# Kernel optimization log

Measured on AMD Instinct MI355X. Metric: run time of the kernel, lower is better.

The kernel has to match this reference:

```python
import jax, jax.numpy as jnp
import numpy as np

N = 100000      # nodes
E = 3200000     # directed edges
F_IN = 128      # input node features
H = 16          # hidden width (fixed by module code)
C = 40          # classes
K_HOPS = 10
ALPHA = 0.1
BN_EPS = 1e-5


def gcn_conv(x, W, b, src, dst, n):
    """PyG GCNConv: add self-loops, symmetric D^-1/2 (A+I) D^-1/2 aggregation of x@W, plus bias."""
    loop = jnp.arange(n)
    s = jnp.concatenate([src, loop])
    d = jnp.concatenate([dst, loop])
    deg = jax.ops.segment_sum(jnp.ones(s.shape[0], x.dtype), d, num_segments=n)
    dinv = jnp.where(deg > 0, jax.lax.rsqrt(deg), 0.0)
    norm = dinv[s] * dinv[d]                      # [E+N]
    h = x @ W                                     # [N, out]
    out = jax.ops.segment_sum(h[s] * norm[:, None], d, num_segments=n)
    return out + b


def setup_inputs() -> dict:
    key = jax.random.key(0)
    ks = jax.random.split(key, 6)
    x = jax.random.normal(ks[0], (N, F_IN), jnp.float32)
    src = jax.random.randint(ks[1], (E,), 0, N)
    dst = jax.random.randint(ks[2], (E,), 0, N)
    glorot = lambda k, sh, fan: jax.random.normal(k, sh, jnp.float32) * np.float32(1.0 / np.sqrt(fan))
    W1 = glorot(ks[3], (F_IN, H), F_IN)
    b1 = jnp.zeros((H,), jnp.float32)
    gamma = jnp.ones((H,), jnp.float32)
    beta = jnp.zeros((H,), jnp.float32)
    Wl = glorot(ks[4], (H, H), H)
    bl = jnp.zeros((H,), jnp.float32)
    W2 = glorot(ks[5], (H, C), H)
    b2 = jnp.zeros((C,), jnp.float32)
    return dict(x=x, src=src, dst=dst, W1=W1, b1=b1, gamma=gamma, beta=beta,
                Wl=Wl, bl=bl, W2=W2, b2=b2)


def reference(x, src, dst, W1, b1, gamma, beta, Wl, bl, W2, b2):
    h = jax.nn.relu(gcn_conv(x, W1, b1, src, dst, N))
    # BatchNorm1d in training mode: biased batch statistics over nodes
    mean = h.mean(axis=0)
    var = h.var(axis=0)
    h = (h - mean) * jax.lax.rsqrt(var + BN_EPS) * gamma + beta
    # k_hops iterations of tiny linear-relu-residual blend
    def step(h, _):
        return ALPHA * jax.nn.relu(h @ Wl + bl) + (1.0 - ALPHA) * h, None
    h, _ = jax.lax.scan(step, h, None, length=K_HOPS)
    out = gcn_conv(h, W2, b2, src, dst, N)
    return jax.nn.log_softmax(out, axis=1)
```

## Files before the change

kernel.cpp:

```cpp
#include <hip/hip_runtime.h>
#include <hip/hip_fp16.h>
#include <math.h>

#define F_IN 128
#define H 16
#define C 40
#define K_HOPS 10
#define ALPHA 0.1f
#define BN_EPS 1e-5f

#define RB 256
#define RB_BITS 8
#define NBKT_MAX 512
#define SRC_MASK 0x1FFFF
#define PADQ 16
#define NDUMMY 2048
#define CAPB_BITS 14
#define CAPB (1 << CAPB_BITS)
#define STAGE_CAP 14336

typedef int v4i __attribute__((ext_vector_type(4)));

__global__ void k_zero(int* __restrict__ gcur, float* __restrict__ stats,
                       __half* __restrict__ h1h, __half* __restrict__ hh, int n) {
    int id = blockIdx.x * blockDim.x + threadIdx.x;
    if (id < NBKT_MAX) gcur[id] = id << CAPB_BITS;
    if (id < 32) stats[id] = 0.0f;
    int* z1 = (int*)(h1h + (size_t)n * H);
    int* z2 = (int*)(hh + (size_t)n * H);
    if (id < NDUMMY * H / 2) { z1[id] = 0; z2[id] = 0; }
}

#define BIN_CHUNK 4096
__global__ __launch_bounds__(512) void k_bin(const int* __restrict__ src,
                                             const int* __restrict__ dst,
                                             int* __restrict__ gcur,
                                             int* __restrict__ temp, int e) {
    __shared__ int hist[NBKT_MAX];
    __shared__ int cur[NBKT_MAX];
    __shared__ int gofs[NBKT_MAX];
    __shared__ int wsum[8];
    __shared__ int stageV[BIN_CHUNK];
    __shared__ int stageD[BIN_CHUNK];
    int t = threadIdx.x;
    hist[t] = 0;
    __syncthreads();
    int base = blockIdx.x * BIN_CHUNK;
    int cnt = e - base; if (cnt > BIN_CHUNK) cnt = BIN_CHUNK;
    const v4i* s4 = reinterpret_cast<const v4i*>(src + base);
    const v4i* d4 = reinterpret_cast<const v4i*>(dst + base);
    v4i sv[2], dv[2];
#pragma unroll
    for (int i = 0; i < 2; ++i) {
        int e0 = (t * 2 + i) * 4;
        if (e0 + 3 < cnt) { sv[i] = s4[t * 2 + i]; dv[i] = d4[t * 2 + i]; }
        else if (e0 < cnt) {
            int ts[4], td[4];
#pragma unroll
            for (int j = 0; j < 4; ++j) {
                int ei = e0 + j;
                ts[j] = (ei < cnt) ? src[base + ei] : 0;
                td[j] = (ei < cnt) ? dst[base + ei] : -1;
            }
            sv[i] = *reinterpret_cast<v4i*>(ts); dv[i] = *reinterpret_cast<v4i*>(td);
        } else { dv[i] = (v4i){-1, -1, -1, -1}; sv[i] = dv[i]; }
    }
#pragma unroll
    for (int i = 0; i < 2; ++i) {
        if (dv[i].x >= 0) atomicAdd(&hist[dv[i].x >> RB_BITS], 1);
        if (dv[i].y >= 0) atomicAdd(&hist[dv[i].y >> RB_BITS], 1);
        if (dv[i].z >= 0) atomicAdd(&hist[dv[i].z >> RB_BITS], 1);
        if (dv[i].w >= 0) atomicAdd(&hist[dv[i].w >> RB_BITS], 1);
    }
    __syncthreads();
    int v = hist[t];
    int lane = t & 63, wv = t >> 6;
    int s = v;
#pragma unroll
    for (int off = 1; off < 64; off <<= 1) { int u = __shfl_up(s, off); if (lane >= off) s += u; }
    if (lane == 63) wsum[wv] = s;
    __syncthreads();
    if (t < 8) {
        int x = wsum[t];
#pragma unroll
        for (int off = 1; off < 8; off <<= 1) { int u = __shfl_up(x, off); if (t >= off) x += u; }
        wsum[t] = x;
    }
    __syncthreads();
    int excl = s - v + (wv ? wsum[wv - 1] : 0);
    cur[t] = excl;
    int g = v ? atomicAdd(&gcur[t], v) : 0;
    gofs[t] = g - excl;
    __syncthreads();
#pragma unroll
    for (int i = 0; i < 2; ++i) {
        int ds[4] = { dv[i].x, dv[i].y, dv[i].z, dv[i].w };
        int ssx[4] = { sv[i].x, sv[i].y, sv[i].z, sv[i].w };
#pragma unroll
        for (int j = 0; j < 4; ++j) {
            int d = ds[j];
            if (d >= 0) {
                int b = d >> RB_BITS;
                int pos = atomicAdd(&cur[b], 1);
                stageV[pos] = ssx[j] | ((d & (RB - 1)) << 17);
                stageD[pos] = gofs[b];
            }
        }
    }
    __syncthreads();
    for (int i = t; i < cnt; i += 512)
        temp[stageD[i] + i] = stageV[i];
}

__global__ __launch_bounds__(512) void k_sort(const int* __restrict__ gcur,
                                              const int* __restrict__ temp,
                                              int* __restrict__ csr,
                                              int* __restrict__ ostart,
                                              int* __restrict__ oend,
                                              int* __restrict__ onode,
                                              float* __restrict__ dinv, int n) {
    __shared__ int hist[RB];
    __shared__ int cur[RB];
    __shared__ int wsum[4];
    __shared__ int qh[64];
    __shared__ int qb[64];
    __shared__ int ptotS;
    __shared__ int stage[STAGE_CAP];
    int t = threadIdx.x;
    int bkt = blockIdx.x;
    int start = bkt << CAPB_BITS;
    int endi = gcur[bkt];
    int nv = endi - start;
    int n4 = nv >> 2;
    const v4i* t4 = reinterpret_cast<const v4i*>(temp + start);
    if (t < RB) hist[t] = 0;
    if (t < 64) qh[t] = 0;
    __syncthreads();
    for (int k = t; k < n4; k += 512) {
        v4i v = t4[k];
        atomicAdd(&hist[v.x >> 17], 1);
        atomicAdd(&hist[v.y >> 17], 1);
        atomicAdd(&hist[v.z >> 17], 1);
        atomicAdd(&hist[v.w >> 17], 1);
    }
    for (int k = start + (n4 << 2) + t; k < endi; k += 512)
        atomicAdd(&hist[temp[k] >> 17], 1);
    __syncthreads();
    int node = (bkt << RB_BITS) + t;
    int h = 0, pv = 0;
    bool va = false;
    if (t < RB) {
        h = hist[t];
        pv = (h + PADQ - 1) & ~(PADQ - 1);
        va = (node < n);
        if (va) dinv[node] = rsqrtf((float)(h + 1));
    }
    int lane = t & 63, wv = t >> 6;
    int s = pv;
#pragma unroll
    for (int off = 1; off < 64; off <<= 1) { int u = __shfl_up(s, off); if (lane >= off) s += u; }
    if (lane == 63 && wv < 4) wsum[wv] = s;
    __syncthreads();
    if (t < 4) {
        int x = wsum[t];
#pragma unroll
        for (int off = 1; off < 4; off <<= 1) { int u = __shfl_up(x, off); if (t >= off) x += u; }
        wsum[t] = x;
        if (t == 3) ptotS = x;
    }
    __syncthreads();
    int pexcl = 0, s0 = 0, q = 63, r = 0;
    if (t < RB) {
        pexcl = s - pv + (wv ? wsum[wv - 1] : 0);
        s0 = start + pexcl;
        q = 63 - min(pv >> 4, 63);
        r = atomicAdd(&qh[q], 1);
    }
    __syncthreads();
    int ptotal = ptotS;
    if (t == 0) {
        int run = 0;
        for (int i = 0; i < 64; ++i) { qb[i] = run; run += qh[i]; }
    }
    __syncthreads();
    if (t < RB) {
        int ga = (bkt << RB_BITS) + qb[q] + r;
        ostart[ga] = s0; oend[ga] = s0 + pv; onode[ga] = va ? node : -1;
    }
    if (ptotal <= STAGE_CAP) {
        if (t < RB) cur[t] = pexcl;
        for (int i = t; i < ptotal; i += 512) stage[i] = -1;
        __syncthreads();
        for (int k = t; k < n4; k += 512) {
            v4i v = t4[k];
            int p0 = atomicAdd(&cur[v.x >> 17], 1); stage[p0] = v.x & SRC_MASK;
            int p1 = atomicAdd(&cur[v.y >> 17], 1); stage[p1] = v.y & SRC_MASK;
            int p2 = atomicAdd(&cur[v.z >> 17], 1); stage[p2] = v.z & SRC_MASK;
            int p3 = atomicAdd(&cur[v.w >> 17], 1); stage[p3] = v.w & SRC_MASK;
        }
        for (int k = start + (n4 << 2) + t; k < endi; k += 512) {
            int v = temp[k];
            int pos = atomicAdd(&cur[v >> 17], 1);
            stage[pos] = v & SRC_MASK;
        }
        __syncthreads();
        for (int i = t * 4; i < ptotal; i += 2048) {
            v4i v = *reinterpret_cast<const v4i*>(&stage[i]);
            int gi = start + i;
            v.x = (v.x < 0) ? n + ((gi + 0) & (NDUMMY - 1)) : v.x;
            v.y = (v.y < 0) ? n + ((gi + 1) & (NDUMMY - 1)) : v.y;
            v.z = (v.z < 0) ? n + ((gi + 2) & (NDUMMY - 1)) : v.z;
            v.w = (v.w < 0) ? n + ((gi + 3) & (NDUMMY - 1)) : v.w;
            *reinterpret_cast<v4i*>(&csr[gi]) = v;
        }
    } else {
        if (t < RB) cur[t] = s0;
        __syncthreads();
        for (int k = start + t; k < endi; k += 512) {
            int v = temp[k];
            int pos = atomicAdd(&cur[v >> 17], 1);
            csr[pos] = v & SRC_MASK;
        }
        __syncthreads();
        if (t < RB) for (int i = s0 + h; i < s0 + pv; ++i) csr[i] = n + (i & (NDUMMY - 1));
    }
}

__global__ __launch_bounds__(256) void k_mm1(const float* __restrict__ x,
                                             const float* __restrict__ W1,
                                             const float* __restrict__ dinv,
                                             __half* __restrict__ h1h, int n) {
    __shared__ __align__(16) float xs[16 * 132];
    __shared__ __align__(16) float ws[128 * 16];
    int t = threadIdx.x;
    int node0 = blockIdx.x * 16;
    const float4* x4 = reinterpret_cast<const float4*>(x);
    const float4* w4 = reinterpret_cast<const float4*>(W1);
#pragma unroll
    for (int r = 0; r < 2; ++r) {
        int f = t + r * 256;
        int nl = f >> 5, k4 = f & 31;
        int nn = node0 + nl; if (nn >= n) nn = n - 1;
        *reinterpret_cast<float4*>(&xs[nl * 132 + k4 * 4]) = x4[(size_t)nn * 32 + k4];
        *reinterpret_cast<float4*>(&ws[f * 4]) = w4[f];
    }
    __syncthreads();
    int nl = t >> 4, j = t & 15;
    float acc = 0.0f;
#pragma unroll 8
    for (int k = 0; k < 128; ++k)
        acc = fmaf(xs[nl * 132 + k], ws[k * 16 + j], acc);
    int node = node0 + nl;
    if (node < n) h1h[(size_t)node * H + j] = __float2half(acc * dinv[node]);
}

__device__ __forceinline__ void acc8(float* a, int4 gv) {
    const __half2* h = reinterpret_cast<const __half2*>(&gv);
    float2 f0 = __half22float2(h[0]);
    float2 f1 = __half22float2(h[1]);
    float2 f2 = __half22float2(h[2]);
    float2 f3 = __half22float2(h[3]);
    a[0] += f0.x; a[1] += f0.y; a[2] += f1.x; a[3] += f1.y;
    a[4] += f2.x; a[5] += f2.y; a[6] += f3.x; a[7] += f3.y;
}

__global__ __launch_bounds__(256) void k_gather1(const int* __restrict__ ostart,
                                                 const int* __restrict__ oend,
                                                 const int* __restrict__ onode,
                                                 const int* __restrict__ csr,
                                                 const __half* __restrict__ h1h,
                                                 const float* __restrict__ dinv,
                                                 const float* __restrict__ b1,
                                                 float* __restrict__ hout,
                                                 float* __restrict__ stats, int n) {
    __shared__ float sm[32];
    __shared__ float b1s[16];
    int t = threadIdx.x;
    if (t < 32) sm[t] = 0.0f;
    if (t < 16) b1s[t] = b1[t];
    __syncthreads();
    int idx = blockIdx.x * 256 + t;
    int g = idx >> 2;
    int L = idx & 3, p = L >> 1, jj = L & 1;
    int node = __builtin_nontemporal_load(onode + g);
    float a[8];
#pragma unroll
    for (int k = 0; k < 8; ++k) a[k] = 0.0f;
    const int4* tab = reinterpret_cast<const int4*>(h1h);
    if (node >= 0) {
        int c  = (__builtin_nontemporal_load(ostart + g) >> 2) + (p << 1);
        int ce = __builtin_nontemporal_load(oend + g) >> 2;
        const v4i* csr4 = reinterpret_cast<const v4i*>(csr);
        for (; c < ce; c += 4) {
            v4i e0 = __builtin_nontemporal_load(csr4 + c);
            v4i e1 = __builtin_nontemporal_load(csr4 + c + 1);
            int4 g0 = tab[(size_t)e0.x * 2 + jj];
            int4 g1 = tab[(size_t)e0.y * 2 + jj];
            int4 g2 = tab[(size_t)e0.z * 2 + jj];
            int4 g3 = tab[(size_t)e0.w * 2 + jj];
            int4 g4 = tab[(size_t)e1.x * 2 + jj];
            int4 g5 = tab[(size_t)e1.y * 2 + jj];
            int4 g6 = tab[(size_t)e1.z * 2 + jj];
            int4 g7 = tab[(size_t)e1.w * 2 + jj];
            acc8(a, g0); acc8(a, g1); acc8(a, g2); acc8(a, g3);
            acc8(a, g4); acc8(a, g5); acc8(a, g6); acc8(a, g7);
        }
    }
#pragma unroll
    for (int k = 0; k < 8; ++k) a[k] += __shfl_xor(a[k], 2);
    float din = 0.0f;
    int4 sv = make_int4(0, 0, 0, 0);
    if (node >= 0) {
        din = dinv[node];
        sv = tab[(size_t)node * 2 + jj];
    }
    float v[8];
    {
        const __half2* h = reinterpret_cast<const __half2*>(&sv);
        float2 f0 = __half22float2(h[0]), f1 = __half22float2(h[1]);
        float2 f2 = __half22float2(h[2]), f3 = __half22float2(h[3]);
        float s8[8] = { f0.x, f0.y, f1.x, f1.y, f2.x, f2.y, f3.x, f3.y };
        bool writer = (node >= 0) && (p == 0);
#pragma unroll
        for (int k = 0; k < 8; ++k) {
            float val = fmaxf(din * (a[k] + s8[k]) + b1s[jj * 8 + k], 0.0f);
            v[k] = writer ? val : 0.0f;
        }
        if (writer) {
            float4* o = reinterpret_cast<float4*>(hout + (size_t)node * H + jj * 8);
            o[0] = make_float4(v[0], v[1], v[2], v[3]);
            o[1] = make_float4(v[4], v[5], v[6], v[7]);
        }
    }
#pragma unroll
    for (int k = 0; k < 8; ++k) {
        float s1 = v[k], s2 = v[k] * v[k];
        s1 += __shfl_xor(s1, 2);  s2 += __shfl_xor(s2, 2);
        s1 += __shfl_xor(s1, 4);  s2 += __shfl_xor(s2, 4);
        s1 += __shfl_xor(s1, 8);  s2 += __shfl_xor(s2, 8);
        s1 += __shfl_xor(s1, 16); s2 += __shfl_xor(s2, 16);
        s1 += __shfl_xor(s1, 32); s2 += __shfl_xor(s2, 32);
        if ((t & 63) < 2) {
            atomicAdd(&sm[jj * 8 + k], s1);
            atomicAdd(&sm[16 + jj * 8 + k], s2);
        }
    }
    __syncthreads();
    if (t < 32) atomicAdd(&stats[t], sm[t]);
}

__global__ __launch_bounds__(256) void k_hops(const float* __restrict__ h,
                                              __half* __restrict__ hh,
                                              const float* __restrict__ stats,
                                              const float* __restrict__ gamma,
                                              const float* __restrict__ beta,
                                              const float* __restrict__ Wl,
                                              const float* __restrict__ bl,
                                              const float* __restrict__ dinv, int n, float nf) {
    __shared__ float wl[256], bls[16], av[16], cv[16];
    int t = threadIdx.x;
    wl[t] = Wl[(t & 15) * 16 + (t >> 4)];
    if (t < 16) {
        bls[t] = bl[t];
        float mean = stats[t] / nf;
        float var = stats[16 + t] / nf - mean * mean;
        float aa = gamma[t] * rsqrtf(var + BN_EPS);
        av[t] = aa;
        cv[t] = beta[t] - mean * aa;
    }
    __syncthreads();
    int node = blockIdx.x * 256 + t;
    if (node >= n) return;
    float hr[16];
    {
        const float4* hp = reinterpret_cast<const float4*>(h + (size_t)node * H);
        float4 v0 = hp[0], v1 = hp[1], v2 = hp[2], v3 = hp[3];
        hr[0] = v0.x; hr[1] = v0.y; hr[2] = v0.z; hr[3] = v0.w;
        hr[4] = v1.x; hr[5] = v1.y; hr[6] = v1.z; hr[7] = v1.w;
        hr[8] = v2.x; hr[9] = v2.y; hr[10] = v2.z; hr[11] = v2.w;
        hr[12] = v3.x; hr[13] = v3.y; hr[14] = v3.z; hr[15] = v3.w;
    }
#pragma unroll
    for (int j = 0; j < 16; ++j) hr[j] = hr[j] * av[j] + cv[j];
    for (int it = 0; it < K_HOPS; ++it) {
        float tmp[16];
#pragma unroll
        for (int j = 0; j < 16; ++j) {
            float a = bls[j];
#pragma unroll
            for (int k = 0; k < 16; ++k) a = fmaf(hr[k], wl[j * 16 + k], a);
            tmp[j] = fmaxf(a, 0.0f);
        }
#pragma unroll
        for (int j = 0; j < 16; ++j) hr[j] = ALPHA * tmp[j] + (1.0f - ALPHA) * hr[j];
    }
    {
        float din = dinv[node];
        __half2 ph[8];
#pragma unroll
        for (int i = 0; i < 8; ++i)
            ph[i] = __floats2half2_rn(hr[2 * i] * din, hr[2 * i + 1] * din);
        int4* hp = reinterpret_cast<int4*>(hh + (size_t)node * H);
        hp[0] = *reinterpret_cast<int4*>(&ph[0]);
        hp[1] = *reinterpret_cast<int4*>(&ph[4]);
    }
}

__global__ __launch_bounds__(256) void k_g2f(const int* __restrict__ ostart,
                                             const int* __restrict__ oend,
                                             const int* __restrict__ onode,
                                             const int* __restrict__ csr,
                                             const __half* __restrict__ hh,
                                             const float* __restrict__ dinv,
                                             const float* __restrict__ W2,
                                             const float* __restrict__ b2,
                                             float* __restrict__ out, int n) {
    __shared__ __align__(16) float w2t[40 * 20];
    __shared__ float b2s[40];
    __shared__ __align__(16) float feat[64 * 20];
    int t = threadIdx.x;
    for (int i = t; i < 640; i += 256) w2t[(i >> 4) * 20 + (i & 15)] = W2[(i & 15) * 40 + (i >> 4)];
    if (t < 40) b2s[t] = b2[t];
    int idx = blockIdx.x * 256 + t;
    int g = idx >> 2;
    int L = idx & 3, p = L >> 1, jj = L & 1;
    int node = __builtin_nontemporal_load(onode + g);
    float a[8];
#pragma unroll
    for (int k = 0; k < 8; ++k) a[k] = 0.0f;
    const int4* tab = reinterpret_cast<const int4*>(hh);
    if (node >= 0) {
        int c  = (__builtin_nontemporal_load(ostart + g) >> 2) + (p << 1);
        int ce = __builtin_nontemporal_load(oend + g) >> 2;
        const v4i* csr4 = reinterpret_cast<const v4i*>(csr);
        for (; c < ce; c += 4) {
            v4i e0 = __builtin_nontemporal_load(csr4 + c);
            v4i e1 = __builtin_nontemporal_load(csr4 + c + 1);
            int4 g0 = tab[(size_t)e0.x * 2 + jj];
            int4 g1 = tab[(size_t)e0.y * 2 + jj];
            int4 g2 = tab[(size_t)e0.z * 2 + jj];
            int4 g3 = tab[(size_t)e0.w * 2 + jj];
            int4 g4 = tab[(size_t)e1.x * 2 + jj];
            int4 g5 = tab[(size_t)e1.y * 2 + jj];
            int4 g6 = tab[(size_t)e1.z * 2 + jj];
            int4 g7 = tab[(size_t)e1.w * 2 + jj];
            acc8(a, g0); acc8(a, g1); acc8(a, g2); acc8(a, g3);
            acc8(a, g4); acc8(a, g5); acc8(a, g6); acc8(a, g7);
        }
    }
#pragma unroll
    for (int k = 0; k < 8; ++k) a[k] += __shfl_xor(a[k], 2);
    int nl = t >> 2;
    if (node >= 0 && p == 0) {
        float din = dinv[node];
        int4 sv = tab[(size_t)node * 2 + jj];
        const __half2* h = reinterpret_cast<const __half2*>(&sv);
        float2 f0 = __half22float2(h[0]), f1 = __half22float2(h[1]);
        float2 f2 = __half22float2(h[2]), f3 = __half22float2(h[3]);
        float s8[8] = { f0.x, f0.y, f1.x, f1.y, f2.x, f2.y, f3.x, f3.y };
        float v[8];
#pragma unroll
        for (int k = 0; k < 8; ++k) v[k] = din * (a[k] + s8[k]);
        *reinterpret_cast<float4*>(&feat[nl * 20 + jj * 8])     = make_float4(v[0], v[1], v[2], v[3]);
        *reinterpret_cast<float4*>(&feat[nl * 20 + jj * 8 + 4]) = make_float4(v[4], v[5], v[6], v[7]);
    }
    __syncthreads();
    float4 f0 = *reinterpret_cast<const float4*>(&feat[nl * 20]);
    float4 f1 = *reinterpret_cast<const float4*>(&feat[nl * 20 + 4]);
    float4 f2 = *reinterpret_cast<const float4*>(&feat[nl * 20 + 8]);
    float4 f3 = *reinterpret_cast<const float4*>(&feat[nl * 20 + 12]);
    int cb = (t & 3) * 10;
    float z[10];
#pragma unroll
    for (int j = 0; j < 10; ++j) {
        const float4* wr = reinterpret_cast<const float4*>(&w2t[(cb + j) * 20]);
        float4 w0 = wr[0], w1 = wr[1], w2v = wr[2], w3 = wr[3];
        float acc = b2s[cb + j];
        acc = fmaf(f0.x, w0.x, acc); acc = fmaf(f0.y, w0.y, acc);
        acc = fmaf(f0.z, w0.z, acc); acc = fmaf(f0.w, w0.w, acc);
        acc = fmaf(f1.x, w1.x, acc); acc = fmaf(f1.y, w1.y, acc);
        acc = fmaf(f1.z, w1.z, acc); acc = fmaf(f1.w, w1.w, acc);
        acc = fmaf(f2.x, w2v.x, acc); acc = fmaf(f2.y, w2v.y, acc);
        acc = fmaf(f2.z, w2v.z, acc); acc = fmaf(f2.w, w2v.w, acc);
        acc = fmaf(f3.x, w3.x, acc); acc = fmaf(f3.y, w3.y, acc);
        acc = fmaf(f3.z, w3.z, acc); acc = fmaf(f3.w, w3.w, acc);
        z[j] = acc;
    }
    float m = z[0];
#pragma unroll
    for (int j = 1; j < 10; ++j) m = fmaxf(m, z[j]);
    m = fmaxf(m, __shfl_xor(m, 1));
    m = fmaxf(m, __shfl_xor(m, 2));
    float s = 0.0f;
#pragma unroll
    for (int j = 0; j < 10; ++j) s += expf(z[j] - m);
    s += __shfl_xor(s, 1);
    s += __shfl_xor(s, 2);
    float lse = m + logf(s);
    if (node >= 0) {
        float2* o = reinterpret_cast<float2*>(out + (size_t)node * 40 + cb);
#pragma unroll
        for (int j = 0; j < 5; ++j)
            o[j] = make_float2(z[2 * j] - lse, z[2 * j + 1] - lse);
    }
}

extern "C" void kernel_launch(void* const* d_in, const int* in_sizes, int n_in,
                              void* d_out, int out_size, void* d_ws, size_t ws_size,
                              hipStream_t stream) {
    const float* x     = (const float*)d_in[0];
    const int*   src   = (const int*)d_in[1];
    const int*   dst   = (const int*)d_in[2];
    const float* W1    = (const float*)d_in[3];
    const float* b1    = (const float*)d_in[4];
    const float* gamma = (const float*)d_in[5];
    const float* beta  = (const float*)d_in[6];
    const float* Wl    = (const float*)d_in[7];
    const float* bl    = (const float*)d_in[8];
    const float* W2    = (const float*)d_in[9];
    const float* b2    = (const float*)d_in[10];
    float* out = (float*)d_out;

    int n = in_sizes[0] / F_IN;
    int e = in_sizes[1];
    int nbkt = (n + RB - 1) >> RB_BITS;
    int nAlign = (n + 15) & ~15;
    int nG = nbkt * RB;
    size_t bktB = (size_t)nbkt << CAPB_BITS;
    size_t hTileB = (size_t)nAlign * H * 4;
    size_t unionB = bktB * 4;
    if (unionB < hTileB) unionB = hTileB;

    char* wsb = (char*)d_ws;
    int*    csr      = (int*)wsb;      wsb += (bktB + 64) * 4;
    char*   uni      = wsb;            wsb += unionB;
    int*    temp     = (int*)uni;
    float*  hbuf     = (float*)uni;
    int*    ostart   = (int*)wsb;      wsb += (size_t)(nG + 16) * 4;
    int*    oend     = (int*)wsb;      wsb += (size_t)(nG + 16) * 4;
    int*    onode    = (int*)wsb;      wsb += (size_t)(nG + 16) * 4;
    float*  dinv     = (float*)wsb;    wsb += (size_t)nAlign * 4;
    int*    gcur     = (int*)wsb;      wsb += NBKT_MAX * 4;
    float*  stats    = (float*)wsb;    wsb += 64 * 4;
    __half* h1h      = (__half*)wsb;   wsb += (size_t)(nAlign + NDUMMY + 16) * H * 2;
    __half* hh       = (__half*)wsb;   wsb += (size_t)(nAlign + NDUMMY + 16) * H * 2;

    k_zero<<<64, 256, 0, stream>>>(gcur, stats, h1h, hh, n);
    k_bin<<<(e + BIN_CHUNK - 1) / BIN_CHUNK, 512, 0, stream>>>(src, dst, gcur, temp, e);
    k_sort<<<nbkt, 512, 0, stream>>>(gcur, temp, csr, ostart, oend, onode, dinv, n);
    k_mm1<<<(n + 15) / 16, 256, 0, stream>>>(x, W1, dinv, h1h, n);
    k_gather1<<<nbkt * 4, 256, 0, stream>>>(ostart, oend, onode, csr, h1h, dinv, b1, hbuf, stats, n);
    k_hops<<<(n + 255) / 256, 256, 0, stream>>>(hbuf, hh, stats, gamma, beta, Wl, bl, dinv, n, (float)n);
    k_g2f<<<nbkt * 4, 256, 0, stream>>>(ostart, oend, onode, csr, hh, dinv, W2, b2, out, n);
}
```

Before: 261.1 us.

## Use persistent grid-stride blocks and prefetch CSR indices in gather kernels

Both gather kernels now launch a fixed grid of 512 blocks that loop over node groups with a grid stride, instead of one block per 64-node group. In the first gather, BN statistics are accumulated in registers across iterations and reduced once per block, which cuts shared and global atomics. The CSR index loads are software-prefetched one iteration ahead so they overlap the feature gathers. k_g2f double-buffers its shared feature tile so only one barrier is needed per iteration. The risks are lower occupancy or load imbalance with only 512 blocks, and extra register pressure from the prefetch.

Result: no change. 264.0 us (+1.1%).

```diff
diff --git a/kernel.cpp b/kernel.cpp
--- a/kernel.cpp
+++ b/kernel.cpp
@@ -18,6 +18,7 @@
 #define CAPB_BITS 14
 #define CAPB (1 << CAPB_BITS)
 #define STAGE_CAP 14336
+#define GR 512
 
 typedef int v4i __attribute__((ext_vector_type(4)));
 
@@ -272,69 +273,78 @@
                                                  const float* __restrict__ dinv,
                                                  const float* __restrict__ b1,
                                                  float* __restrict__ hout,
-                                                 float* __restrict__ stats, int n) {
+                                                 float* __restrict__ stats, int nG, int n) {
     __shared__ float sm[32];
     __shared__ float b1s[16];
     int t = threadIdx.x;
     if (t < 32) sm[t] = 0.0f;
     if (t < 16) b1s[t] = b1[t];
     __syncthreads();
-    int idx = blockIdx.x * 256 + t;
-    int g = idx >> 2;
-    int L = idx & 3, p = L >> 1, jj = L & 1;
-    int node = __builtin_nontemporal_load(onode + g);
-    float a[8];
-#pragma unroll
-    for (int k = 0; k < 8; ++k) a[k] = 0.0f;
+    int L = t & 3, p = L >> 1, jj = L & 1;
     const int4* tab = reinterpret_cast<const int4*>(h1h);
-    if (node >= 0) {
-        int c  = (__builtin_nontemporal_load(ostart + g) >> 2) + (p << 1);
-        int ce = __builtin_nontemporal_load(oend + g) >> 2;
-        const v4i* csr4 = reinterpret_cast<const v4i*>(csr);
-        for (; c < ce; c += 4) {
-            v4i e0 = __builtin_nontemporal_load(csr4 + c);
-            v4i e1 = __builtin_nontemporal_load(csr4 + c + 1);
-            int4 g0 = tab[(size_t)e0.x * 2 + jj];
-            int4 g1 = tab[(size_t)e0.y * 2 + jj];
-            int4 g2 = tab[(size_t)e0.z * 2 + jj];
-            int4 g3 = tab[(size_t)e0.w * 2 + jj];
-            int4 g4 = tab[(size_t)e1.x * 2 + jj];
-            int4 g5 = tab[(size_t)e1.y * 2 + jj];
-            int4 g6 = tab[(size_t)e1.z * 2 + jj];
-            int4 g7 = tab[(size_t)e1.w * 2 + jj];
-            acc8(a, g0); acc8(a, g1); acc8(a, g2); acc8(a, g3);
-            acc8(a, g4); acc8(a, g5); acc8(a, g6); acc8(a, g7);
-        }
-    }
-#pragma unroll
-    for (int k = 0; k < 8; ++k) a[k] += __shfl_xor(a[k], 2);
-    float din = 0.0f;
-    int4 sv = make_int4(0, 0, 0, 0);
-    if (node >= 0) {
-        din = dinv[node];
-        sv = tab[(size_t)node * 2 + jj];
-    }
-    float v[8];
-    {
-        const __half2* h = reinterpret_cast<const __half2*>(&sv);
-        float2 f0 = __half22float2(h[0]), f1 = __half22float2(h[1]);
-        float2 f2 = __half22float2(h[2]), f3 = __half22float2(h[3]);
-        float s8[8] = { f0.x, f0.y, f1.x, f1.y, f2.x, f2.y, f3.x, f3.y };
-        bool writer = (node >= 0) && (p == 0);
-#pragma unroll
-        for (int k = 0; k < 8; ++k) {
-            float val = fmaxf(din * (a[k] + s8[k]) + b1s[jj * 8 + k], 0.0f);
-            v[k] = writer ? val : 0.0f;
-        }
-        if (writer) {
-            float4* o = reinterpret_cast<float4*>(hout + (size_t)node * H + jj * 8);
-            o[0] = make_float4(v[0], v[1], v[2], v[3]);
-            o[1] = make_float4(v[4], v[5], v[6], v[7]);
+    const v4i* csr4 = reinterpret_cast<const v4i*>(csr);
+    float bs1[8], bs2[8];
+#pragma unroll
+    for (int k = 0; k < 8; ++k) { bs1[k] = 0.0f; bs2[k] = 0.0f; }
+    for (int gBase = blockIdx.x * 64; gBase < nG; gBase += GR * 64) {
+        int g = gBase + (t >> 2);
+        int node = __builtin_nontemporal_load(onode + g);
+        float a[8];
+#pragma unroll
+        for (int k = 0; k < 8; ++k) a[k] = 0.0f;
+        if (node >= 0) {
+            int c  = (__builtin_nontemporal_load(ostart + g) >> 2) + (p << 1);
+            int ce = __builtin_nontemporal_load(oend + g) >> 2;
+            v4i e0 = (v4i){0, 0, 0, 0}, e1 = e0;
+            if (c < ce) { e0 = __builtin_nontemporal_load(csr4 + c); e1 = __builtin_nontemporal_load(csr4 + c + 1); }
+            while (c < ce) {
+                v4i f0 = e0, f1 = e1;
+                c += 4;
+                if (c < ce) { e0 = __builtin_nontemporal_load(csr4 + c); e1 = __builtin_nontemporal_load(csr4 + c + 1); }
+                int4 g0 = tab[(size_t)f0.x * 2 + jj];
+                int4 g1 = tab[(size_t)f0.y * 2 + jj];
+                int4 g2 = tab[(size_t)f0.z * 2 + jj];
+                int4 g3 = tab[(size_t)f0.w * 2 + jj];
+                int4 g4 = tab[(size_t)f1.x * 2 + jj];
+                int4 g5 = tab[(size_t)f1.y * 2 + jj];
+                int4 g6 = tab[(size_t)f1.z * 2 + jj];
+                int4 g7 = tab[(size_t)f1.w * 2 + jj];
+                acc8(a, g0); acc8(a, g1); acc8(a, g2); acc8(a, g3);
+                acc8(a, g4); acc8(a, g5); acc8(a, g6); acc8(a, g7);
+            }
+        }
+#pragma unroll
+        for (int k = 0; k < 8; ++k) a[k] += __shfl_xor(a[k], 2);
+        float din = 0.0f;
+        int4 sv = make_int4(0, 0, 0, 0);
+        if (node >= 0) {
+            din = dinv[node];
+            sv = tab[(size_t)node * 2 + jj];
+        }
+        {
+            const __half2* h = reinterpret_cast<const __half2*>(&sv);
+            float2 f0 = __half22float2(h[0]), f1 = __half22float2(h[1]);
+            float2 f2 = __half22float2(h[2]), f3 = __half22float2(h[3]);
+            float s8[8] = { f0.x, f0.y, f1.x, f1.y, f2.x, f2.y, f3.x, f3.y };
+            bool writer = (node >= 0) && (p == 0);
+            float v[8];
+#pragma unroll
+            for (int k = 0; k < 8; ++k) {
+                float val = fmaxf(din * (a[k] + s8[k]) + b1s[jj * 8 + k], 0.0f);
+                v[k] = writer ? val : 0.0f;
+                bs1[k] += v[k];
+                bs2[k] += v[k] * v[k];
+            }
+            if (writer) {
+                float4* o = reinterpret_cast<float4*>(hout + (size_t)node * H + jj * 8);
+                o[0] = make_float4(v[0], v[1], v[2], v[3]);
+                o[1] = make_float4(v[4], v[5], v[6], v[7]);
+            }
         }
     }
 #pragma unroll
     for (int k = 0; k < 8; ++k) {
-        float s1 = v[k], s2 = v[k] * v[k];
+        float s1 = bs1[k], s2 = bs2[k];
         s1 += __shfl_xor(s1, 2);  s2 += __shfl_xor(s2, 2);
         s1 += __shfl_xor(s1, 4);  s2 += __shfl_xor(s2, 4);
         s1 += __shfl_xor(s1, 8);  s2 += __shfl_xor(s2, 8);
@@ -414,94 +424,99 @@
                                              const float* __restrict__ dinv,
                                              const float* __restrict__ W2,
                                              const float* __restrict__ b2,
-                                             float* __restrict__ out, int n) {
+                                             float* __restrict__ out, int nG, int n) {
     __shared__ __align__(16) float w2t[40 * 20];
     __shared__ float b2s[40];
-    __shared__ __align__(16) float feat[64 * 20];
+    __shared__ __align__(16) float feat[2][64 * 20];
     int t = threadIdx.x;
     for (int i = t; i < 640; i += 256) w2t[(i >> 4) * 20 + (i & 15)] = W2[(i & 15) * 40 + (i >> 4)];
     if (t < 40) b2s[t] = b2[t];
-    int idx = blockIdx.x * 256 + t;
-    int g = idx >> 2;
-    int L = idx & 3, p = L >> 1, jj = L & 1;
-    int node = __builtin_nontemporal_load(onode + g);
-    float a[8];
-#pragma unroll
-    for (int k = 0; k < 8; ++k) a[k] = 0.0f;
+    int L = t & 3, p = L >> 1, jj = L & 1;
+    int nl = t >> 2;
+    int cb = (t & 3) * 10;
     const int4* tab = reinterpret_cast<const int4*>(hh);
-    if (node >= 0) {
-        int c  = (__builtin_nontemporal_load(ostart + g) >> 2) + (p << 1);
-        int ce = __builtin_nontemporal_load(oend + g) >> 2;
-        const v4i* csr4 = reinterpret_cast<const v4i*>(csr);
-        for (; c < ce; c += 4) {
-            v4i e0 = __builtin_nontemporal_load(csr4 + c);
-            v4i e1 = __builtin_nontemporal_load(csr4 + c + 1);
-            int4 g0 = tab[(size_t)e0.x * 2 + jj];
-            int4 g1 = tab[(size_t)e0.y * 2 + jj];
-            int4 g2 = tab[(size_t)e0.z * 2 + jj];
-            int4 g3 = tab[(size_t)e0.w * 2 + jj];
-            int4 g4 = tab[(size_t)e1.x * 2 + jj];
-            int4 g5 = tab[(size_t)e1.y * 2 + jj];
-            int4 g6 = tab[(size_t)e1.z * 2 + jj];
-            int4 g7 = tab[(size_t)e1.w * 2 + jj];
-            acc8(a, g0); acc8(a, g1); acc8(a, g2); acc8(a, g3);
-            acc8(a, g4); acc8(a, g5); acc8(a, g6); acc8(a, g7);
-        }
-    }
-#pragma unroll
-    for (int k = 0; k < 8; ++k) a[k] += __shfl_xor(a[k], 2);
-    int nl = t >> 2;
-    if (node >= 0 && p == 0) {
-        float din = dinv[node];
-        int4 sv = tab[(size_t)node * 2 + jj];
-        const __half2* h = reinterpret_cast<const __half2*>(&sv);
-        float2 f0 = __half22float2(h[0]), f1 = __half22float2(h[1]);
-        float2 f2 = __half22float2(h[2]), f3 = __half22float2(h[3]);
-        float s8[8] = { f0.x, f0.y, f1.x, f1.y, f2.x, f2.y, f3.x, f3.y };
-        float v[8];
-#pragma unroll
-        for (int k = 0; k < 8; ++k) v[k] = din * (a[k] + s8[k]);
-        *reinterpret_cast<float4*>(&feat[nl * 20 + jj * 8])     = make_float4(v[0], v[1], v[2], v[3]);
-        *reinterpret_cast<float4*>(&feat[nl * 20 + jj * 8 + 4]) = make_float4(v[4], v[5], v[6], v[7]);
-    }
-    __syncthreads();
-    float4 f0 = *reinterpret_cast<const float4*>(&feat[nl * 20]);
-    float4 f1 = *reinterpret_cast<const float4*>(&feat[nl * 20 + 4]);
-    float4 f2 = *reinterpret_cast<const float4*>(&feat[nl * 20 + 8]);
-    float4 f3 = *reinterpret_cast<const float4*>(&feat[nl * 20 + 12]);
-    int cb = (t & 3) * 10;
-    float z[10];
-#pragma unroll
-    for (int j = 0; j < 10; ++j) {
-        const float4* wr = reinterpret_cast<const float4*>(&w2t[(cb + j) * 20]);
-        float4 w0 = wr[0], w1 = wr[1], w2v = wr[2], w3 = wr[3];
-        float acc = b2s[cb + j];
-        acc = fmaf(f0.x, w0.x, acc); acc = fmaf(f0.y, w0.y, acc);
-        acc = fmaf(f0.z, w0.z, acc); acc = fmaf(f0.w, w0.w, acc);
-        acc = fmaf(f1.x, w1.x, acc); acc = fmaf(f1.y, w1.y, acc);
-        acc = fmaf(f1.z, w1.z, acc); acc = fmaf(f1.w, w1.w, acc);
-        acc = fmaf(f2.x, w2v.x, acc); acc = fmaf(f2.y, w2v.y, acc);
-        acc = fmaf(f2.z, w2v.z, acc); acc = fmaf(f2.w, w2v.w, acc);
-        acc = fmaf(f3.x, w3.x, acc); acc = fmaf(f3.y, w3.y, acc);
-        acc = fmaf(f3.z, w3.z, acc); acc = fmaf(f3.w, w3.w, acc);
-        z[j] = acc;
-    }
-    float m = z[0];
-#pragma unroll
-    for (int j = 1; j < 10; ++j) m = fmaxf(m, z[j]);
-    m = fmaxf(m, __shfl_xor(m, 1));
-    m = fmaxf(m, __shfl_xor(m, 2));
-    float s = 0.0f;
-#pragma unroll
-    for (int j = 0; j < 10; ++j) s += expf(z[j] - m);
-    s += __shfl_xor(s, 1);
-    s += __shfl_xor(s, 2);
-    float lse = m + logf(s);
-    if (node >= 0) {
-        float2* o = reinterpret_cast<float2*>(out + (size_t)node * 40 + cb);
-#pragma unroll
-        for (int j = 0; j < 5; ++j)
-            o[j] = make_float2(z[2 * j] - lse, z[2 * j + 1] - lse);
+    const v4i* csr4 = reinterpret_cast<const v4i*>(csr);
+    int buf = 0;
+    for (int gBase = blockIdx.x * 64; gBase < nG; gBase += GR * 64, buf ^= 1) {
+        int g = gBase + nl;
+        int node = __builtin_nontemporal_load(onode + g);
+        float a[8];
+#pragma unroll
+        for (int k = 0; k < 8; ++k) a[k] = 0.0f;
+        if (node >= 0) {
+            int c  = (__builtin_nontemporal_load(ostart + g) >> 2) + (p << 1);
+            int ce = __builtin_nontemporal_load(oend + g) >> 2;
+            v4i e0 = (v4i){0, 0, 0, 0}, e1 = e0;
+            if (c < ce) { e0 = __builtin_nontemporal_load(csr4 + c); e1 = __builtin_nontemporal_load(csr4 + c + 1); }
+            while (c < ce) {
+                v4i f0 = e0, f1 = e1;
+                c += 4;
+                if (c < ce) { e0 = __builtin_nontemporal_load(csr4 + c); e1 = __builtin_nontemporal_load(csr4 + c + 1); }
+                int4 g0 = tab[(size_t)f0.x * 2 + jj];
+                int4 g1 = tab[(size_t)f0.y * 2 + jj];
+                int4 g2 = tab[(size_t)f0.z * 2 + jj];
+                int4 g3 = tab[(size_t)f0.w * 2 + jj];
+                int4 g4 = tab[(size_t)f1.x * 2 + jj];
+                int4 g5 = tab[(size_t)f1.y * 2 + jj];
+                int4 g6 = tab[(size_t)f1.z * 2 + jj];
+                int4 g7 = tab[(size_t)f1.w * 2 + jj];
+                acc8(a, g0); acc8(a, g1); acc8(a, g2); acc8(a, g3);
+                acc8(a, g4); acc8(a, g5); acc8(a, g6); acc8(a, g7);
+            }
+        }
+#pragma unroll
+        for (int k = 0; k < 8; ++k) a[k] += __shfl_xor(a[k], 2);
+        if (node >= 0 && p == 0) {
+            float din = dinv[node];
+            int4 sv = tab[(size_t)node * 2 + jj];
+            const __half2* h = reinterpret_cast<const __half2*>(&sv);
+            float2 f0 = __half22float2(h[0]), f1 = __half22float2(h[1]);
+            float2 f2 = __half22float2(h[2]), f3 = __half22float2(h[3]);
+            float s8[8] = { f0.x, f0.y, f1.x, f1.y, f2.x, f2.y, f3.x, f3.y };
+            float v[8];
+#pragma unroll
+            for (int k = 0; k < 8; ++k) v[k] = din * (a[k] + s8[k]);
+            *reinterpret_cast<float4*>(&feat[buf][nl * 20 + jj * 8])     = make_float4(v[0], v[1], v[2], v[3]);
+            *reinterpret_cast<float4*>(&feat[buf][nl * 20 + jj * 8 + 4]) = make_float4(v[4], v[5], v[6], v[7]);
+        }
+        __syncthreads();
+        float4 f0 = *reinterpret_cast<const float4*>(&feat[buf][nl * 20]);
+        float4 f1 = *reinterpret_cast<const float4*>(&feat[buf][nl * 20 + 4]);
+        float4 f2 = *reinterpret_cast<const float4*>(&feat[buf][nl * 20 + 8]);
+        float4 f3 = *reinterpret_cast<const float4*>(&feat[buf][nl * 20 + 12]);
+        float z[10];
+#pragma unroll
+        for (int j = 0; j < 10; ++j) {
+            const float4* wr = reinterpret_cast<const float4*>(&w2t[(cb + j) * 20]);
+            float4 w0 = wr[0], w1 = wr[1], w2v = wr[2], w3 = wr[3];
+            float acc = b2s[cb + j];
+            acc = fmaf(f0.x, w0.x, acc); acc = fmaf(f0.y, w0.y, acc);
+            acc = fmaf(f0.z, w0.z, acc); acc = fmaf(f0.w, w0.w, acc);
+            acc = fmaf(f1.x, w1.x, acc); acc = fmaf(f1.y, w1.y, acc);
+            acc = fmaf(f1.z, w1.z, acc); acc = fmaf(f1.w, w1.w, acc);
+            acc = fmaf(f2.x, w2v.x, acc); acc = fmaf(f2.y, w2v.y, acc);
+            acc = fmaf(f2.z, w2v.z, acc); acc = fmaf(f2.w, w2v.w, acc);
+            acc = fmaf(f3.x, w3.x, acc); acc = fmaf(f3.y, w3.y, acc);
+            acc = fmaf(f3.z, w3.z, acc); acc = fmaf(f3.w, w3.w, acc);
+            z[j] = acc;
+        }
+        float m = z[0];
+#pragma unroll
+        for (int j = 1; j < 10; ++j) m = fmaxf(m, z[j]);
+        m = fmaxf(m, __shfl_xor(m, 1));
+        m = fmaxf(m, __shfl_xor(m, 2));
+        float s = 0.0f;
+#pragma unroll
+        for (int j = 0; j < 10; ++j) s += expf(z[j] - m);
+        s += __shfl_xor(s, 1);
+        s += __shfl_xor(s, 2);
+        float lse = m + logf(s);
+        if (node >= 0) {
+            float2* o = reinterpret_cast<float2*>(out + (size_t)node * 40 + cb);
+#pragma unroll
+            for (int j = 0; j < 5; ++j)
+                o[j] = make_float2(z[2 * j] - lse, z[2 * j + 1] - lse);
+        }
     }
 }
 
@@ -549,7 +564,7 @@
     k_bin<<<(e + BIN_CHUNK - 1) / BIN_CHUNK, 512, 0, stream>>>(src, dst, gcur, temp, e);
     k_sort<<<nbkt, 512, 0, stream>>>(gcur, temp, csr, ostart, oend, onode, dinv, n);
     k_mm1<<<(n + 15) / 16, 256, 0, stream>>>(x, W1, dinv, h1h, n);
-    k_gather1<<<nbkt * 4, 256, 0, stream>>>(ostart, oend, onode, csr, h1h, dinv, b1, hbuf, stats, n);
+    k_gather1<<<GR, 256, 0, stream>>>(ostart, oend, onode, csr, h1h, dinv, b1, hbuf, stats, nG, n);
     k_hops<<<(n + 255) / 256, 256, 0, stream>>>(hbuf, hh, stats, gamma, beta, Wl, bl, dinv, n, (float)n);
-    k_g2f<<<nbkt * 4, 256, 0, stream>>>(ostart, oend, onode, csr, hh, dinv, W2, b2, out, n);
-}
+    k_g2f<<<GR, 256, 0, stream>>>(ostart, oend, onode, csr, hh, dinv, W2, b2, out, nG, n);
+}
```
